# Performance work log

Hardware: AMD Instinct MI355X
Metric: run time of the kernel (lower is better)

Reference implementation:

```python
import jax, jax.numpy as jnp
import numpy as np

EMB_DIM = 512
N_HEAD = 8
EPS = 1e-5


def gen_pos_emb(emb_dim, max_len):
    half = emb_dim // 2
    r = 10000.0 ** (-1.0 / half)
    freq = r ** jnp.arange(half, dtype=jnp.float32)  # cumprod of [1, r, r, ...]
    phase = jnp.arange(max_len, dtype=jnp.float32)[:, None] * freq[None, :]  # [L, half]
    pe = jnp.zeros((max_len, emb_dim), dtype=jnp.float32)
    pe = pe.at[:, 0::2].set(jnp.sin(phase)).at[:, 1::2].set(jnp.cos(phase))
    return pe  # [L, E]


def setup_inputs() -> dict:
    key = jax.random.key(0)
    ks = jax.random.split(key, 12)
    bs, L, E, H, V = 8, 2048, EMB_DIM, N_HEAD, 32000
    inputs = jax.random.randint(ks[0], (bs, L), 0, V, dtype=jnp.int64 if jax.config.jax_enable_x64 else jnp.int32)
    lens = jnp.sort(jax.random.randint(ks[1], (bs,), 1, L + 1, dtype=jnp.int32))
    lens = lens.at[-1].set(L)  # model requires lens[-1] == max_len
    s = 0.02
    emb_table = (jax.random.normal(ks[2], (V, E), jnp.float32) * s).at[0].set(0.0)  # padding_idx=0
    qkv_w = jax.random.normal(ks[3], (3 * E, E), jnp.float32) * s
    qkv_b = jax.random.normal(ks[4], (3 * E,), jnp.float32) * s
    gn_w = jnp.ones((H,), jnp.float32)
    gn_b = jnp.zeros((H,), jnp.float32)
    ln_w = jnp.ones((E,), jnp.float32)
    ln_b = jnp.zeros((E,), jnp.float32)
    w1 = jax.random.normal(ks[5], (2 * E, E), jnp.float32) * s
    b1 = jax.random.normal(ks[6], (2 * E,), jnp.float32) * s
    w2 = jax.random.normal(ks[7], (E, 2 * E), jnp.float32) * s
    b2 = jax.random.normal(ks[8], (E,), jnp.float32) * s
    return {"inputs": inputs, "lens": lens, "emb_table": emb_table, "qkv_w": qkv_w,
            "qkv_b": qkv_b, "gn_w": gn_w, "gn_b": gn_b, "ln_w": ln_w, "ln_b": ln_b,
            "w1": w1, "b1": b1, "w2": w2, "b2": b2}


def _forward(inputs, lens, emb_table, qkv_w, qkv_b, gn_w, gn_b, ln_w, ln_b, w1, b1, w2, b2):
    bs, L = inputs.shape
    E, H = EMB_DIM, N_HEAD
    dh = E // H
    scaling = (E / H) ** -0.5

    # embedding + positional encoding; torch works seq-major: emb [L, bs, E]
    emb = emb_table[inputs.T] + gen_pos_emb(E, L)[:, None, :]

    # qkv projection and head split
    qkv = emb @ qkv_w.T + qkv_b                      # [L, bs, 3E]
    qkv = qkv.reshape(L, bs * H, 3 * dh).transpose(1, 0, 2)  # [B=bs*H, L, 3dh]
    q, k, v = jnp.split(qkv, 3, axis=-1)             # each [B, L, dh]

    # attention-sum: softmax over keys with zero-score mask, then sum over queries
    scores = jnp.einsum('bqd,bkd->bqk', q, k) * scaling   # [B, L, L]
    mask = scores == 0
    aw = jax.nn.softmax(jnp.where(mask, -jnp.inf, scores), axis=-1)
    aw = jnp.where(mask, 0.0, aw).sum(axis=-2)            # [B, L]

    attn_out = jnp.einsum('bl,bld->bd', aw, v).reshape(bs, H, dh)  # [bs, H, dh]

    # GroupNorm(n_head, n_head): per-channel normalization over dh with affine
    mu = attn_out.mean(-1, keepdims=True)
    var = attn_out.var(-1, keepdims=True)
    attn_out = (attn_out - mu) * jax.lax.rsqrt(var + EPS)
    attn_out = attn_out * gn_w[None, :, None] + gn_b[None, :, None]
    ft = attn_out.reshape(bs, E)

    # post_process: residual with length-normalized sum of embeddings
    x = ft + emb.sum(0) / lens.astype(emb.dtype)[:, None]  # [bs, E]

    # LayerNorm -> Linear -> tanh -> Linear, residual
    m = x.mean(-1, keepdims=True)
    vv = x.var(-1, keepdims=True)
    xn = (x - m) * jax.lax.rsqrt(vv + EPS) * ln_w + ln_b
    ff = jnp.tanh(xn @ w1.T + b1) @ w2.T + b2
    return x + ff


def reference(inputs, lens, emb_table, qkv_w, qkv_b, gn_w, gn_b, ln_w, ln_b, w1, b1, w2, b2):
    return _forward(inputs, lens, emb_table, qkv_w, qkv_b, gn_w, gn_b, ln_w, ln_b, w1, b1, w2, b2)
```

## Files before the change

kernel.cpp:

```cpp
#include <hip/hip_runtime.h>
#include <math.h>

#define L_SEQ 2048
#define BS 8
#define EMB 512
#define NHEAD 8
#define DH 64
#define NB (BS*NHEAD)
#define SCALE_Q 0.18033688f

typedef short short8  __attribute__((ext_vector_type(8)));
typedef short short4v __attribute__((ext_vector_type(4)));
typedef float f32x4   __attribute__((ext_vector_type(4)));

__device__ __forceinline__ short f2bf(float x) {
    unsigned u = __float_as_uint(x);
    unsigned r = (u + 0x7FFFu + ((u >> 16) & 1u)) >> 16;
    return (short)r;
}
__device__ __forceinline__ float bf2f(short h) {
    return __uint_as_float(((unsigned)(unsigned short)h) << 16);
}

__global__ void freq_kernel(float* __restrict__ freq) {
    int j = threadIdx.x;
    double r = pow(10000.0, -1.0 / 256.0);
    float rf = (float)r;
    freq[j] = (float)pow((double)rf, (double)j);
}

__global__ __launch_bounds__(256) void pe_kernel(const float* __restrict__ freq,
                                                 float* __restrict__ pe) {
    int l = blockIdx.x;
    int j = threadIdx.x;
    float ph = (float)l * freq[j];
    pe[l*EMB + 2*j]     = sinf(ph);
    pe[l*EMB + 2*j + 1] = cosf(ph);
}

__global__ __launch_bounds__(256) void embed_kernel(const int* __restrict__ inputs,
                                                    const float* __restrict__ table,
                                                    const float* __restrict__ pe,
                                                    float* __restrict__ emb,
                                                    short* __restrict__ ahi,
                                                    short* __restrict__ alo) {
    int idx = blockIdx.x*256 + threadIdx.x;
    int e4 = idx & 127;
    int rb = idx >> 7;
    int b  = rb & 7;
    int l  = rb >> 3;
    int tok = inputs[b*L_SEQ + l];
    float4 tv = reinterpret_cast<const float4*>(table)[(size_t)tok*128 + e4];
    float4 pv = reinterpret_cast<const float4*>(pe)[(size_t)l*128 + e4];
    float4 o;
    o.x = tv.x + pv.x; o.y = tv.y + pv.y; o.z = tv.z + pv.z; o.w = tv.w + pv.w;
    reinterpret_cast<float4*>(emb)[(size_t)rb*128 + e4] = o;
    int e0   = e4 * 4;
    int tile = rb >> 4;
    int ks   = e0 >> 5;
    int lane = (rb & 15) + (((e0 >> 3) & 3) << 4);
    int j0   = e0 & 7;
    size_t off = ((((size_t)tile*16 + ks) << 6) + lane)*8 + j0;
    float v[4] = {o.x, o.y, o.z, o.w};
    short4v h4, l4;
    #pragma unroll
    for (int q = 0; q < 4; q++) {
        short hb = f2bf(v[q]);
        h4[q] = hb;
        l4[q] = f2bf(v[q] - bf2f(hb));
    }
    *reinterpret_cast<short4v*>(ahi + off) = h4;
    *reinterpret_cast<short4v*>(alo + off) = l4;
}

__global__ __launch_bounds__(256) void embsum_kernel(const float* __restrict__ emb,
                                                     float* __restrict__ embsum) {
    int b  = blockIdx.x;
    int ec = blockIdx.y;
    int lc = blockIdx.z;
    int e  = ec*256 + threadIdx.x;
    float s = 0.f;
    int l0 = lc*128;
    for (int l = l0; l < l0+128; l++)
        s += emb[((size_t)l*BS + b)*EMB + e];
    atomicAdd(&embsum[b*EMB + e], s);
}

__global__ __launch_bounds__(256) void wsplit_kernel(const float* __restrict__ src,
                                                     short8* __restrict__ hi,
                                                     short8* __restrict__ lo) {
    int idx = blockIdx.x*256 + threadIdx.x;
    int c = idx & 63;
    int r = idx >> 6;
    const float4* s4 = reinterpret_cast<const float4*>(src + (size_t)r*512 + c*8);
    float4 f0 = s4[0], f1 = s4[1];
    int ks   = c >> 2;
    int lane = (r & 15) + ((c & 3) << 4);
    int tile = r >> 4;
    float v[8] = {f0.x,f0.y,f0.z,f0.w,f1.x,f1.y,f1.z,f1.w};
    short8 h8, l8;
    #pragma unroll
    for (int q = 0; q < 8; q++) {
        short hb = f2bf(v[q]);
        h8[q] = hb;
        l8[q] = f2bf(v[q] - bf2f(hb));
    }
    size_t o = (((size_t)tile*16 + ks) << 6) + lane;
    hi[o] = h8; lo[o] = l8;
}

__global__ __launch_bounds__(256) void qkv_mfma_kernel(const short8* __restrict__ ahi,
                                                       const short8* __restrict__ alo,
                                                       const short8* __restrict__ bhi,
                                                       const short8* __restrict__ blo,
                                                       const float* __restrict__ bias,
                                                       short* __restrict__ qbf_s,
                                                       short* __restrict__ kbf_s,
                                                       float* __restrict__ vg) {
    __shared__ short8 sA[2][8][64];
    __shared__ short8 sB[2][8][64];
    int id  = blockIdx.x;
    int xcd = id & 7, pos = id >> 3;
    int nb  = pos % 12;
    int mb  = xcd*16 + pos/12;
    int t  = threadIdx.x;
    int w  = t >> 6, lane = t & 63;
    int wr = w >> 1, wc = w & 1;

    f32x4 acc[4][4];
    #pragma unroll
    for (int i = 0; i < 4; i++)
        #pragma unroll
        for (int j = 0; j < 4; j++)
            acc[i][j] = (f32x4){0.f, 0.f, 0.f, 0.f};

    short8 stg[8];
    #pragma unroll
    for (int i = 0; i < 8; i++) {
        int li = w*8 + i;
        int h = li & 1, ti = (li >> 1) & 7, isB = li >> 4;
        const short8* base = isB ? (h ? blo : bhi) : (h ? alo : ahi);
        int gt = isB ? (nb*8 + ti) : (mb*8 + ti);
        stg[i] = base[(((size_t)gt*16 + 0) << 6) + lane];
    }
    for (int ks = 0; ks < 16; ks++) {
        __syncthreads();
        #pragma unroll
        for (int i = 0; i < 8; i++) {
            int li = w*8 + i;
            int h = li & 1, ti = (li >> 1) & 7, isB = li >> 4;
            if (isB) sB[h][ti][lane] = stg[i];
            else     sA[h][ti][lane] = stg[i];
        }
        __syncthreads();
        if (ks < 15) {
            #pragma unroll
            for (int i = 0; i < 8; i++) {
                int li = w*8 + i;
                int h = li & 1, ti = (li >> 1) & 7, isB = li >> 4;
                const short8* base = isB ? (h ? blo : bhi) : (h ? alo : ahi);
                int gt = isB ? (nb*8 + ti) : (mb*8 + ti);
                stg[i] = base[(((size_t)gt*16 + (ks+1)) << 6) + lane];
            }
        }
        short8 Ah[4], Al[4];
        #pragma unroll
        for (int fi = 0; fi < 4; fi++) {
            Ah[fi] = sA[0][wr*4 + fi][lane];
            Al[fi] = sA[1][wr*4 + fi][lane];
        }
        #pragma unroll
        for (int fj = 0; fj < 4; fj++) {
            short8 Bh = sB[0][wc*4 + fj][lane];
            short8 Bl = sB[1][wc*4 + fj][lane];
            #pragma unroll
            for (int fi = 0; fi < 4; fi++) {
                acc[fi][fj] = __builtin_amdgcn_mfma_f32_16x16x32_bf16(Ah[fi], Bh, acc[fi][fj], 0, 0, 0);
                acc[fi][fj] = __builtin_amdgcn_mfma_f32_16x16x32_bf16(Ah[fi], Bl, acc[fi][fj], 0, 0, 0);
                acc[fi][fj] = __builtin_amdgcn_mfma_f32_16x16x32_bf16(Al[fi], Bh, acc[fi][fj], 0, 0, 0);
            }
        }
    }
    int row0 = (lane >> 4) * 4;
    int col  = lane & 15;
    #pragma unroll
    for (int fj = 0; fj < 4; fj++) {
        int n   = nb*128 + wc*64 + fj*16 + col;
        int h   = n / 192;
        int sel = (n % 192) / 64;
        float bn = bias[n];
        int nn = n & 63;
        #pragma unroll
        for (int fi = 0; fi < 4; fi++) {
            int m0 = mb*128 + wr*64 + fi*16 + row0;
            #pragma unroll
            for (int r = 0; r < 4; r++) {
                int m = m0 + r;
                int l = m >> 3, b = m & 7;
                float val = acc[fi][fj][r] + bn;
                if (sel == 2) {
                    vg[(((size_t)(b*NHEAD + h))*L_SEQ + l)*DH + nn] = val;
                } else {
                    int bh   = b*NHEAD + h;
                    int tile = l >> 4;
                    int kss  = nn >> 5;
                    int ln2  = (l & 15) + (((nn >> 3) & 3) << 4);
                    size_t off = ((((size_t)(bh*128 + tile)*2 + kss) << 6) + ln2)*8 + (nn & 7);
                    if (sel == 1) kbf_s[off] = f2bf(val);
                    else          qbf_s[off] = f2bf(val * SCALE_Q);
                }
            }
        }
    }
}

__global__ __launch_bounds__(256) void ml_mfma_kernel(const short8* __restrict__ qbf,
                                                      const short8* __restrict__ kbf,
                                                      float* __restrict__ cq) {
    int bh = blockIdx.x, wv = threadIdx.x >> 6, lane = threadIdx.x & 63;
    int z  = blockIdx.z;
    int qt0 = (blockIdx.y*4 + wv)*4;
    short8 bq0[4], bq1[4];
    #pragma unroll
    for (int j = 0; j < 4; j++) {
        const short8* qp = qbf + (((size_t)(bh*128 + qt0 + j)*2) << 6) + lane;
        bq0[j] = qp[0]; bq1[j] = qp[64];
    }
    const short8* kp = kbf + ((size_t)bh << 14) + lane + (size_t)z*4096;
    float lsum[4] = {0.f, 0.f, 0.f, 0.f};
    for (int t = 0; t < 32; t++) {
        short8 a0 = kp[0], a1 = kp[64];
        kp += 128;
        #pragma unroll
        for (int j = 0; j < 4; j++) {
            f32x4 acc = {0.f, 0.f, 0.f, 0.f};
            acc = __builtin_amdgcn_mfma_f32_16x16x32_bf16(a0, bq0[j], acc, 0, 0, 0);
            acc = __builtin_amdgcn_mfma_f32_16x16x32_bf16(a1, bq1[j], acc, 0, 0, 0);
            #pragma unroll
            for (int r = 0; r < 4; r++)
                lsum[j] += (acc[r] != 0.f) ? __builtin_amdgcn_exp2f(acc[r]) : 0.f;
        }
    }
    #pragma unroll
    for (int j = 0; j < 4; j++) {
        lsum[j] += __shfl_xor(lsum[j], 16);
        lsum[j] += __shfl_xor(lsum[j], 32);
    }
    if (lane < 16) {
        #pragma unroll
        for (int j = 0; j < 4; j++)
            atomicAdd(&cq[(size_t)bh*L_SEQ + (qt0+j)*16 + lane], lsum[j]);
    }
}

__global__ __launch_bounds__(256) void kw_mfma_kernel(const short8* __restrict__ qbf,
                                                      const short8* __restrict__ kbf,
                                                      const float* __restrict__ cq,
                                                      float* __restrict__ wk) {
    int bh = blockIdx.x, wv = threadIdx.x >> 6, lane = threadIdx.x & 63;
    int z  = blockIdx.z;
    int kt0 = (blockIdx.y*4 + wv)*4;
    short8 bk0[4], bk1[4];
    #pragma unroll
    for (int j = 0; j < 4; j++) {
        const short8* kp = kbf + (((size_t)(bh*128 + kt0 + j)*2) << 6) + lane;
        bk0[j] = kp[0]; bk1[j] = kp[64];
    }
    const short8* qp = qbf + ((size_t)bh << 14) + lane + (size_t)z*4096;
    const float4* cp = reinterpret_cast<const float4*>(cq + (size_t)bh*L_SEQ) + (lane >> 4) + z*128;
    float w[4] = {0.f, 0.f, 0.f, 0.f};
    for (int t = 0; t < 32; t++) {
        short8 a0 = qp[0], a1 = qp[64];
        qp += 128;
        float4 c4 = cp[0]; cp += 4;
        float cr[4];
        cr[0] = (c4.x > 0.f) ? __builtin_amdgcn_rcpf(c4.x) : 0.f;
        cr[1] = (c4.y > 0.f) ? __builtin_amdgcn_rcpf(c4.y) : 0.f;
        cr[2] = (c4.z > 0.f) ? __builtin_amdgcn_rcpf(c4.z) : 0.f;
        cr[3] = (c4.w > 0.f) ? __builtin_amdgcn_rcpf(c4.w) : 0.f;
        #pragma unroll
        for (int j = 0; j < 4; j++) {
            f32x4 acc = {0.f, 0.f, 0.f, 0.f};
            acc = __builtin_amdgcn_mfma_f32_16x16x32_bf16(a0, bk0[j], acc, 0, 0, 0);
            acc = __builtin_amdgcn_mfma_f32_16x16x32_bf16(a1, bk1[j], acc, 0, 0, 0);
            #pragma unroll
            for (int r = 0; r < 4; r++) {
                float p = __builtin_amdgcn_exp2f(acc[r]);
                w[j] += (acc[r] != 0.f) ? p*cr[r] : 0.f;
            }
        }
    }
    #pragma unroll
    for (int j = 0; j < 4; j++) {
        w[j] += __shfl_xor(w[j], 16);
        w[j] += __shfl_xor(w[j], 32);
    }
    if (lane < 16) {
        #pragma unroll
        for (int j = 0; j < 4; j++)
            atomicAdd(&wk[(size_t)bh*L_SEQ + (kt0+j)*16 + lane], w[j]);
    }
}

__global__ __launch_bounds__(256) void pv_kernel(const float* __restrict__ vg,
                                                 const float* __restrict__ wk,
                                                 float* __restrict__ O) {
    __shared__ float red[256];
    int bidx = blockIdx.x;
    int seg  = blockIdx.y;
    int t    = threadIdx.x;
    int d    = t & 63;
    int ks   = t >> 6;
    const float* vrow = vg + ((size_t)bidx*L_SEQ + seg*256)*DH;
    const float* wrow = wk + (size_t)bidx*L_SEQ + seg*256;
    float acc = 0.f;
    for (int k = ks; k < 256; k += 4)
        acc += wrow[k] * vrow[k*64 + d];
    red[t] = acc;
    __syncthreads();
    if (t < 128) red[t] += red[t + 128];
    __syncthreads();
    if (t < 64) atomicAdd(&O[bidx*64 + t], red[t] + red[t + 64]);
}

__global__ __launch_bounds__(256) void ln_kernel(const float* __restrict__ O,
                                                 const float* __restrict__ embsum,
                                                 const int* __restrict__ lens,
                                                 const float* __restrict__ gn_w,
                                                 const float* __restrict__ gn_b,
                                                 const float* __restrict__ ln_w,
                                                 const float* __restrict__ ln_b,
                                                 float* __restrict__ xbuf,
                                                 float* __restrict__ xnbuf) {
    int b = blockIdx.x;
    int t = threadIdx.x;
    __shared__ float x[EMB];
    __shared__ float rbuf[16];
    {
        int h = t >> 5;
        int i32 = t & 31;
        float v0 = O[b*EMB + h*64 + i32];
        float v1 = O[b*EMB + h*64 + i32 + 32];
        float s = v0+v1, ss = v0*v0 + v1*v1;
        #pragma unroll
        for (int off = 16; off >= 1; off >>= 1) {
            s  += __shfl_xor(s,  off, 32);
            ss += __shfl_xor(ss, off, 32);
        }
        float mu  = s * (1.f/64.f);
        float var = ss * (1.f/64.f) - mu*mu;
        float rstd = rsqrtf(var + 1e-5f);
        float gw = gn_w[h], gb = gn_b[h];
        float len = (float)lens[b];
        x[h*64+i32]    = (v0-mu)*rstd*gw + gb + embsum[b*EMB + h*64+i32] / len;
        x[h*64+i32+32] = (v1-mu)*rstd*gw + gb + embsum[b*EMB + h*64+i32+32] / len;
    }
    __syncthreads();
    float xv0 = x[t], xv1 = x[t+256];
    {
        float s = xv0+xv1, ss = xv0*xv0 + xv1*xv1;
        #pragma unroll
        for (int off = 32; off >= 1; off >>= 1) {
            s  += __shfl_xor(s,  off);
            ss += __shfl_xor(ss, off);
        }
        int wid = t >> 6;
        if ((t & 63) == 0) { rbuf[wid] = s; rbuf[8+wid] = ss; }
        __syncthreads();
        float S  = rbuf[0]+rbuf[1]+rbuf[2]+rbuf[3];
        float SS = rbuf[8]+rbuf[9]+rbuf[10]+rbuf[11];
        float mu  = S * (1.f/512.f);
        float var = SS * (1.f/512.f) - mu*mu;
        float rstd = rsqrtf(var + 1e-5f);
        xnbuf[b*EMB + t]       = (xv0-mu)*rstd*ln_w[t]     + ln_b[t];
        xnbuf[b*EMB + t + 256] = (xv1-mu)*rstd*ln_w[t+256] + ln_b[t+256];
        xbuf[b*EMB + t]        = xv0;
        xbuf[b*EMB + t + 256]  = xv1;
    }
}

__global__ __launch_bounds__(256) void mlp1_kernel(const float* __restrict__ xnbuf,
                                                   const float* __restrict__ w1,
                                                   const float* __restrict__ b1,
                                                   float* __restrict__ h1buf) {
    __shared__ float sxn[BS][EMB];
    int t = threadIdx.x;
    #pragma unroll
    for (int i = 0; i < 4; i++)
        reinterpret_cast<float4*>(&sxn[0][0])[t + 256*i] =
            reinterpret_cast<const float4*>(xnbuf)[t + 256*i];
    __syncthreads();
    int b = t & 7;
    int j = blockIdx.x*32 + (t >> 3);
    const float4* wr = reinterpret_cast<const float4*>(w1 + (size_t)j*512);
    const float4* xr = reinterpret_cast<const float4*>(&sxn[b][0]);
    float a0 = 0.f, a1 = 0.f;
    #pragma unroll 8
    for (int i = 0; i < 128; i += 2) {
        float4 wv = wr[i],   xv = xr[i];
        a0 += wv.x*xv.x + wv.y*xv.y + wv.z*xv.z + wv.w*xv.w;
        float4 wv1 = wr[i+1], xv1 = xr[i+1];
        a1 += wv1.x*xv1.x + wv1.y*xv1.y + wv1.z*xv1.z + wv1.w*xv1.w;
    }
    h1buf[b*1024 + j] = tanhf(a0 + a1 + b1[j]);
}

__global__ __launch_bounds__(256) void mlp2_kernel(const float* __restrict__ h1buf,
                                                   const float* __restrict__ xbuf,
                                                   const float* __restrict__ w2,
                                                   const float* __restrict__ b2,
                                                   float* __restrict__ out) {
    __shared__ float sh1[BS][2*EMB];
    int t = threadIdx.x;
    #pragma unroll
    for (int i = 0; i < 8; i++)
        reinterpret_cast<float4*>(&sh1[0][0])[t + 256*i] =
            reinterpret_cast<const float4*>(h1buf)[t + 256*i];
    __syncthreads();
    int b = t & 7;
    int e = blockIdx.x*32 + (t >> 3);
    const float4* wr = reinterpret_cast<const float4*>(w2 + (size_t)e*1024);
    const float4* hr = reinterpret_cast<const float4*>(&sh1[b][0]);
    float a0 = 0.f, a1 = 0.f;
    #pragma unroll 8
    for (int i = 0; i < 256; i += 2) {
        float4 wv = wr[i],   hv = hr[i];
        a0 += wv.x*hv.x + wv.y*hv.y + wv.z*hv.z + wv.w*hv.w;
        float4 wv1 = wr[i+1], hv1 = hr[i+1];
        a1 += wv1.x*hv1.x + wv1.y*hv1.y + wv1.z*hv1.z + wv1.w*hv1.w;
    }
    out[b*EMB + e] = xbuf[b*EMB + e] + a0 + a1 + b2[e];
}

extern "C" void kernel_launch(void* const* d_in, const int* in_sizes, int n_in,
                              void* d_out, int out_size, void* d_ws, size_t ws_size,
                              hipStream_t stream) {
    const int*   inputs    = (const int*)d_in[0];
    const int*   lens      = (const int*)d_in[1];
    const float* emb_table = (const float*)d_in[2];
    const float* qkv_w     = (const float*)d_in[3];
    const float* qkv_b     = (const float*)d_in[4];
    const float* gn_w      = (const float*)d_in[5];
    const float* gn_b      = (const float*)d_in[6];
    const float* ln_w      = (const float*)d_in[7];
    const float* ln_b      = (const float*)d_in[8];
    const float* w1        = (const float*)d_in[9];
    const float* b1        = (const float*)d_in[10];
    const float* w2        = (const float*)d_in[11];
    const float* b2        = (const float*)d_in[12];
    float* out = (float*)d_out;

    float* ws = (float*)d_ws;
    const size_t NE = (size_t)L_SEQ*BS*EMB;
    float* emb    = ws;
    float* vg     = emb + NE;
    float* pe     = vg  + NE;
    float* afrag  = pe  + (size_t)L_SEQ*EMB;
    short* ahi_s  = reinterpret_cast<short*>(afrag);
    short* alo_s  = ahi_s + NE;
    float* qkrows = afrag + NE;
    float* wfrag  = qkrows + NE;
    short8* bhi   = reinterpret_cast<short8*>(wfrag);
    short8* blo   = bhi + 98304;
    float* cqbuf  = wfrag + 786432;
    float* wkbuf  = cqbuf + (size_t)NB*L_SEQ;
    float* freq   = wkbuf + (size_t)NB*L_SEQ;
    float* embsum = freq + 256;
    float* Oacc   = embsum + BS*EMB;
    float* xbuf   = Oacc + NB*DH;
    float* xnbuf  = xbuf + BS*EMB;
    float* h1buf  = xnbuf + BS*EMB;
    short8* kbf = reinterpret_cast<short8*>(emb);
    short8* qbf = kbf + (size_t)NB*128*2*64;

    hipMemsetAsync(cqbuf, 0, (2*(size_t)NB*L_SEQ + 256 + 2*BS*EMB) * sizeof(float), stream);

    freq_kernel<<<1, 256, 0, stream>>>(freq);
    pe_kernel<<<L_SEQ, 256, 0, stream>>>(freq, pe);
    embed_kernel<<<(L_SEQ*BS*(EMB/4))/256, 256, 0, stream>>>(inputs, emb_table, pe, emb,
                                                             ahi_s, alo_s);
    embsum_kernel<<<dim3(BS, 2, 16), 256, 0, stream>>>(emb, embsum);
    wsplit_kernel<<<384, 256, 0, stream>>>(qkv_w, bhi, blo);
    qkv_mfma_kernel<<<1536, 256, 0, stream>>>(reinterpret_cast<const short8*>(ahi_s),
                                              reinterpret_cast<const short8*>(alo_s),
                                              bhi, blo, qkv_b,
                                              reinterpret_cast<short*>(qbf),
                                              reinterpret_cast<short*>(kbf), vg);
    ml_mfma_kernel<<<dim3(NB, 8, 4), 256, 0, stream>>>(qbf, kbf, cqbuf);
    kw_mfma_kernel<<<dim3(NB, 8, 4), 256, 0, stream>>>(qbf, kbf, cqbuf, wkbuf);
    pv_kernel<<<dim3(NB, 8), 256, 0, stream>>>(vg, wkbuf, Oacc);
    ln_kernel<<<BS, 256, 0, stream>>>(Oacc, embsum, lens, gn_w, gn_b, ln_w, ln_b, xbuf, xnbuf);
    mlp1_kernel<<<32, 256, 0, stream>>>(xnbuf, w1, b1, h1buf);
    mlp2_kernel<<<16, 256, 0, stream>>>(h1buf, xbuf, w2, b2, out);
}
```

Baseline: 400.9 us.

## Fuse embedding-sum into embed kernel and drop low-bf16 activation split in QKV GEMM

The embed kernel now accumulates the per-batch embedding sum directly, with a shared-memory reduction followed by atomics, so the fp32 emb buffer is no longer written and the separate embsum kernel is removed. Activations are stored only as a single bf16 high part, which removes the alo buffer and one of the three split-precision MFMAs per tile in the QKV GEMM. This cuts memory traffic and matrix work, but lowers activation precision in the projection to plain bf16, which could affect accuracy.

```diff
diff --git a/kernel.cpp b/kernel.cpp
--- a/kernel.cpp
+++ b/kernel.cpp
@@ -41,49 +41,53 @@
 __global__ __launch_bounds__(256) void embed_kernel(const int* __restrict__ inputs,
                                                     const float* __restrict__ table,
                                                     const float* __restrict__ pe,
-                                                    float* __restrict__ emb,
                                                     short* __restrict__ ahi,
-                                                    short* __restrict__ alo) {
-    int idx = blockIdx.x*256 + threadIdx.x;
-    int e4 = idx & 127;
-    int rb = idx >> 7;
-    int b  = rb & 7;
-    int l  = rb >> 3;
-    int tok = inputs[b*L_SEQ + l];
-    float4 tv = reinterpret_cast<const float4*>(table)[(size_t)tok*128 + e4];
-    float4 pv = reinterpret_cast<const float4*>(pe)[(size_t)l*128 + e4];
-    float4 o;
-    o.x = tv.x + pv.x; o.y = tv.y + pv.y; o.z = tv.z + pv.z; o.w = tv.w + pv.w;
-    reinterpret_cast<float4*>(emb)[(size_t)rb*128 + e4] = o;
-    int e0   = e4 * 4;
-    int tile = rb >> 4;
-    int ks   = e0 >> 5;
-    int lane = (rb & 15) + (((e0 >> 3) & 3) << 4);
-    int j0   = e0 & 7;
-    size_t off = ((((size_t)tile*16 + ks) << 6) + lane)*8 + j0;
-    float v[4] = {o.x, o.y, o.z, o.w};
-    short4v h4, l4;
-    #pragma unroll
-    for (int q = 0; q < 4; q++) {
-        short hb = f2bf(v[q]);
-        h4[q] = hb;
-        l4[q] = f2bf(v[q] - bf2f(hb));
-    }
-    *reinterpret_cast<short4v*>(ahi + off) = h4;
-    *reinterpret_cast<short4v*>(alo + off) = l4;
-}
-
-__global__ __launch_bounds__(256) void embsum_kernel(const float* __restrict__ emb,
-                                                     float* __restrict__ embsum) {
+                                                    float* __restrict__ embsum) {
+    __shared__ float4 red[32][8];
     int b  = blockIdx.x;
-    int ec = blockIdx.y;
-    int lc = blockIdx.z;
-    int e  = ec*256 + threadIdx.x;
-    float s = 0.f;
-    int l0 = lc*128;
-    for (int l = l0; l < l0+128; l++)
-        s += emb[((size_t)l*BS + b)*EMB + e];
-    atomicAdd(&embsum[b*EMB + e], s);
+    int lc = blockIdx.y;
+    int ec = blockIdx.z;
+    int t  = threadIdx.x;
+    int e4l  = t & 31;
+    int lsub = t >> 5;
+    int e4 = ec*32 + e4l;
+    int e0 = e4*4;
+    int ks = e0 >> 5;
+    int lanehi = ((e0 >> 3) & 3) << 4;
+    int j0 = e0 & 7;
+    float4 sum = {0.f, 0.f, 0.f, 0.f};
+    #pragma unroll 4
+    for (int i = 0; i < 16; i++) {
+        int l = lc*128 + lsub*16 + i;
+        int tok = inputs[b*L_SEQ + l];
+        float4 tv = reinterpret_cast<const float4*>(table)[(size_t)tok*128 + e4];
+        float4 pv = reinterpret_cast<const float4*>(pe)[(size_t)l*128 + e4];
+        float4 o;
+        o.x = tv.x + pv.x; o.y = tv.y + pv.y; o.z = tv.z + pv.z; o.w = tv.w + pv.w;
+        sum.x += o.x; sum.y += o.y; sum.z += o.z; sum.w += o.w;
+        int m = l*BS + b;
+        int tile = m >> 4;
+        int lane = (m & 15) + lanehi;
+        size_t off = ((((size_t)tile*16 + ks) << 6) + lane)*8 + j0;
+        short4v h4;
+        h4[0] = f2bf(o.x); h4[1] = f2bf(o.y); h4[2] = f2bf(o.z); h4[3] = f2bf(o.w);
+        *reinterpret_cast<short4v*>(ahi + off) = h4;
+    }
+    red[e4l][lsub] = sum;
+    __syncthreads();
+    if (t < 32) {
+        float4 s = red[t][0];
+        #pragma unroll
+        for (int i = 1; i < 8; i++) {
+            float4 v = red[t][i];
+            s.x += v.x; s.y += v.y; s.z += v.z; s.w += v.w;
+        }
+        int e = ec*128 + t*4;
+        atomicAdd(&embsum[b*EMB + e + 0], s.x);
+        atomicAdd(&embsum[b*EMB + e + 1], s.y);
+        atomicAdd(&embsum[b*EMB + e + 2], s.z);
+        atomicAdd(&embsum[b*EMB + e + 3], s.w);
+    }
 }
 
 __global__ __launch_bounds__(256) void wsplit_kernel(const float* __restrict__ src,
@@ -110,14 +114,13 @@
 }
 
 __global__ __launch_bounds__(256) void qkv_mfma_kernel(const short8* __restrict__ ahi,
-                                                       const short8* __restrict__ alo,
                                                        const short8* __restrict__ bhi,
                                                        const short8* __restrict__ blo,
                                                        const float* __restrict__ bias,
                                                        short* __restrict__ qbf_s,
                                                        short* __restrict__ kbf_s,
                                                        float* __restrict__ vg) {
-    __shared__ short8 sA[2][8][64];
+    __shared__ short8 sA[8][64];
     __shared__ short8 sB[2][8][64];
     int id  = blockIdx.x;
     int xcd = id & 7, pos = id >> 3;
@@ -134,41 +137,46 @@
         for (int j = 0; j < 4; j++)
             acc[i][j] = (f32x4){0.f, 0.f, 0.f, 0.f};
 
-    short8 stg[8];
-    #pragma unroll
-    for (int i = 0; i < 8; i++) {
-        int li = w*8 + i;
-        int h = li & 1, ti = (li >> 1) & 7, isB = li >> 4;
-        const short8* base = isB ? (h ? blo : bhi) : (h ? alo : ahi);
-        int gt = isB ? (nb*8 + ti) : (mb*8 + ti);
-        stg[i] = base[(((size_t)gt*16 + 0) << 6) + lane];
+    short8 stg[6];
+    #pragma unroll
+    for (int i = 0; i < 6; i++) {
+        int li = w*6 + i;
+        const short8* p;
+        if (li < 8) p = &ahi[((((size_t)(mb*8 + li))*16 + 0) << 6) + lane];
+        else {
+            int idx = li - 8;
+            const short8* base = (idx & 1) ? blo : bhi;
+            p = &base[((((size_t)(nb*8 + (idx >> 1)))*16 + 0) << 6) + lane];
+        }
+        stg[i] = *p;
     }
     for (int ks = 0; ks < 16; ks++) {
         __syncthreads();
         #pragma unroll
-        for (int i = 0; i < 8; i++) {
-            int li = w*8 + i;
-            int h = li & 1, ti = (li >> 1) & 7, isB = li >> 4;
-            if (isB) sB[h][ti][lane] = stg[i];
-            else     sA[h][ti][lane] = stg[i];
+        for (int i = 0; i < 6; i++) {
+            int li = w*6 + i;
+            if (li < 8) sA[li][lane] = stg[i];
+            else { int idx = li - 8; sB[idx & 1][idx >> 1][lane] = stg[i]; }
         }
         __syncthreads();
         if (ks < 15) {
             #pragma unroll
-            for (int i = 0; i < 8; i++) {
-                int li = w*8 + i;
-                int h = li & 1, ti = (li >> 1) & 7, isB = li >> 4;
-                const short8* base = isB ? (h ? blo : bhi) : (h ? alo : ahi);
-                int gt = isB ? (nb*8 + ti) : (mb*8 + ti);
-                stg[i] = base[(((size_t)gt*16 + (ks+1)) << 6) + lane];
+            for (int i = 0; i < 6; i++) {
+                int li = w*6 + i;
+                const short8* p;
+                if (li < 8) p = &ahi[((((size_t)(mb*8 + li))*16 + (ks+1)) << 6) + lane];
+                else {
+                    int idx = li - 8;
+                    const short8* base = (idx & 1) ? blo : bhi;
+                    p = &base[((((size_t)(nb*8 + (idx >> 1)))*16 + (ks+1)) << 6) + lane];
+                }
+                stg[i] = *p;
             }
         }
-        short8 Ah[4], Al[4];
-        #pragma unroll
-        for (int fi = 0; fi < 4; fi++) {
-            Ah[fi] = sA[0][wr*4 + fi][lane];
-            Al[fi] = sA[1][wr*4 + fi][lane];
-        }
+        short8 Ah[4];
+        #pragma unroll
+        for (int fi = 0; fi < 4; fi++)
+            Ah[fi] = sA[wr*4 + fi][lane];
         #pragma unroll
         for (int fj = 0; fj < 4; fj++) {
             short8 Bh = sB[0][wc*4 + fj][lane];
@@ -177,7 +185,6 @@
             for (int fi = 0; fi < 4; fi++) {
                 acc[fi][fj] = __builtin_amdgcn_mfma_f32_16x16x32_bf16(Ah[fi], Bh, acc[fi][fj], 0, 0, 0);
                 acc[fi][fj] = __builtin_amdgcn_mfma_f32_16x16x32_bf16(Ah[fi], Bl, acc[fi][fj], 0, 0, 0);
-                acc[fi][fj] = __builtin_amdgcn_mfma_f32_16x16x32_bf16(Al[fi], Bh, acc[fi][fj], 0, 0, 0);
             }
         }
     }
@@ -457,7 +464,6 @@
     float* pe     = vg  + NE;
     float* afrag  = pe  + (size_t)L_SEQ*EMB;
     short* ahi_s  = reinterpret_cast<short*>(afrag);
-    short* alo_s  = ahi_s + NE;
     float* qkrows = afrag + NE;
     float* wfrag  = qkrows + NE;
     short8* bhi   = reinterpret_cast<short8*>(wfrag);
@@ -477,12 +483,9 @@
 
     freq_kernel<<<1, 256, 0, stream>>>(freq);
     pe_kernel<<<L_SEQ, 256, 0, stream>>>(freq, pe);
-    embed_kernel<<<(L_SEQ*BS*(EMB/4))/256, 256, 0, stream>>>(inputs, emb_table, pe, emb,
-                                                             ahi_s, alo_s);
-    embsum_kernel<<<dim3(BS, 2, 16), 256, 0, stream>>>(emb, embsum);
+    embed_kernel<<<dim3(BS, 16, 4), 256, 0, stream>>>(inputs, emb_table, pe, ahi_s, embsum);
     wsplit_kernel<<<384, 256, 0, stream>>>(qkv_w, bhi, blo);
     qkv_mfma_kernel<<<1536, 256, 0, stream>>>(reinterpret_cast<const short8*>(ahi_s),
-                                              reinterpret_cast<const short8*>(alo_s),
                                               bhi, blo, qkv_b,
                                               reinterpret_cast<short*>(qbf),
                                               reinterpret_cast<short*>(kbf), vg);
```

Measured after the change: 389.5 us. 2.8% less time.
